# Performance work log

Measured on AMD Instinct MI355X. Metric: run time of the kernel, lower is better.

The kernel has to match this reference:

```python
import jax, jax.numpy as jnp
import numpy as np

N_NODES, N_EDGES, N_GRAPHS, D = 32768, 49152, 1024, 64


def setup_inputs() -> dict:
    key = jax.random.key(0)
    ks = jax.random.split(key, 24)
    p = lambda k, shape, s=0.1: jax.random.normal(k, shape, dtype=jnp.float32) * s
    return dict(
        x=jax.random.normal(ks[0], (N_NODES, 14), dtype=jnp.float32),
        edge_index=jax.random.randint(ks[1], (2, N_EDGES), 0, N_NODES),
        edge_attr=jax.random.uniform(ks[2], (N_EDGES, 4), dtype=jnp.float32),
        batch=jnp.sort(jax.random.randint(ks[3], (N_NODES,), 0, N_GRAPHS)),
        lin0_W=p(ks[4], (D, 14)), lin0_b=p(ks[5], (D,)),
        e1_W=p(ks[6], (128, 4)), e1_b=p(ks[7], (128,)),
        e2_W=p(ks[8], (D * D, 128), 0.02), e2_b=p(ks[9], (D * D,), 0.02),
        root_W=p(ks[10], (D, D)), conv_b=p(ks[11], (D,)),
        gru_Wih=p(ks[12], (3 * D, D)), gru_Whh=p(ks[13], (3 * D, D)),
        gru_bih=p(ks[14], (3 * D,)), gru_bhh=p(ks[15], (3 * D,)),
        lstm_Wih=p(ks[16], (4 * D, 2 * D)), lstm_Whh=p(ks[17], (4 * D, D)),
        lstm_bih=p(ks[18], (4 * D,)), lstm_bhh=p(ks[19], (4 * D,)),
        fc1_W=p(ks[20], (128, 2 * D)), fc1_b=p(ks[21], (128,)),
        fc2_W=p(ks[22], (1, 128)), fc2_b=p(ks[23], (1,)),
    )


def reference(x, edge_index, edge_attr, batch,
              lin0_W, lin0_b, e1_W, e1_b, e2_W, e2_b, root_W, conv_b,
              gru_Wih, gru_Whh, gru_bih, gru_bhh,
              lstm_Wih, lstm_Whh, lstm_bih, lstm_bhh,
              fc1_W, fc1_b, fc2_W, fc2_b):
    N, B = x.shape[0], N_GRAPHS
    src, dst = edge_index[0], edge_index[1]

    out = jax.nn.relu(x @ lin0_W.T + lin0_b)            # [N, D]
    h = out                                             # GRU hidden (num_layers=1)

    # Edge-conditioned weights: edge_attr is constant across the 3 iterations,
    # so compute the edge MLP once (identical math to re-running it).
    W = jax.nn.relu(edge_attr @ e1_W.T + e1_b) @ e2_W.T + e2_b
    W = W.reshape(-1, D, D)                             # [E, D, D]
    cnt = jnp.maximum(
        jax.ops.segment_sum(jnp.ones((src.shape[0],), x.dtype), dst, num_segments=N), 1.0)

    for _ in range(3):
        # NNConv (aggr='mean'): gather -> per-edge matmul -> scatter-mean -> root + bias
        msg = jnp.einsum('ei,eio->eo', out[src], W)     # [E, D]
        agg = jax.ops.segment_sum(msg, dst, num_segments=N) / cnt[:, None]
        m = jax.nn.relu(agg + out @ root_W + conv_b)
        # GRU cell (seq_len=1)
        gi = m @ gru_Wih.T + gru_bih
        gh = h @ gru_Whh.T + gru_bhh
        ir, iz, inn = jnp.split(gi, 3, -1)
        hr, hz, hn = jnp.split(gh, 3, -1)
        r = jax.nn.sigmoid(ir + hr)
        z = jax.nn.sigmoid(iz + hz)
        n = jnp.tanh(inn + r * hn)
        h = (1.0 - z) * n + z * h
        out = h

    # Set2Set pooling, 3 processing steps, LSTM(2D -> D)
    q_star = jnp.zeros((B, 2 * D), x.dtype)
    hl = jnp.zeros((B, D), x.dtype)
    cl = jnp.zeros((B, D), x.dtype)
    for _ in range(3):
        g = q_star @ lstm_Wih.T + lstm_bih + hl @ lstm_Whh.T + lstm_bhh
        i_, f_, g_, o_ = jnp.split(g, 4, -1)
        cl = jax.nn.sigmoid(f_) * cl + jax.nn.sigmoid(i_) * jnp.tanh(g_)
        hl = jax.nn.sigmoid(o_) * jnp.tanh(cl)
        q = hl                                          # [B, D]
        e = jnp.sum(out * q[batch], -1)                 # [N]
        mx = jax.ops.segment_max(e, batch, num_segments=B)
        ex = jnp.exp(e - mx[batch])
        den = jax.ops.segment_sum(ex, batch, num_segments=B)
        a = ex / den[batch]                             # segment softmax
        r_read = jax.ops.segment_sum(a[:, None] * out, batch, num_segments=B)
        q_star = jnp.concatenate([q, r_read], -1)       # [B, 2D]

    hid = jax.nn.relu(q_star @ fc1_W.T + fc1_b)
    return hid @ fc2_W.T + fc2_b                        # [B, 1]
```

## Files before the change

kernel.cpp:

```cpp
#include <hip/hip_runtime.h>
#include <math.h>

#define NN_ 32768
#define NE_ 49152
#define NG_ 1024

typedef short bh8 __attribute__((ext_vector_type(8)));
typedef float f32x4 __attribute__((ext_vector_type(4)));

__device__ __forceinline__ unsigned short f2bfu(float f) {
    union { float f; unsigned int i; } x; x.f = f;
    unsigned int u = x.i;
    u += 0x7FFFu + ((u >> 16) & 1u);
    return (unsigned short)(u >> 16);
}
__device__ __forceinline__ float sigm(float x) { return 1.f / (1.f + expf(-x)); }

__global__ void MPNN_78632261256134_kernel() {}

__global__ void k_init(int* deg, float* agg) {
    int i = blockIdx.x * 256 + threadIdx.x;
    if (i < NN_) deg[i] = 0;
    int k = i - NN_;
    if (k >= 0 && k < NN_ * 64) agg[k] = 0.f;
}

__global__ void k_lin0(const float* x, const float* W, const float* b, float* node) {
    int g = blockIdx.x * 256 + threadIdx.x;
    int n = g >> 6, d = g & 63;
    const float* xr = x + n * 14;
    const float* wr = W + d * 14;
    float acc = b[d];
    for (int i = 0; i < 14; i++) acc += xr[i] * wr[i];
    node[g] = fmaxf(acc, 0.f);
}

__global__ void k_cnt(const int* dst, int* deg) {
    int e = blockIdx.x * 256 + threadIdx.x;
    if (e < NE_) atomicAdd(&deg[dst[e]], 1);
}

__global__ __launch_bounds__(256) void k_scanA(const int* __restrict__ deg,
                                               int* __restrict__ offs,
                                               int* __restrict__ bsum) {
    __shared__ int wtot[4];
    int tid = threadIdx.x, bid = blockIdx.x;
    int i = bid * 256 + tid;
    int v = deg[i];
    int sc = v;
    for (int o = 1; o < 64; o <<= 1) { int u = __shfl_up(sc, o); if ((tid & 63) >= o) sc += u; }
    if ((tid & 63) == 63) wtot[tid >> 6] = sc;
    __syncthreads();
    int wpre = 0;
    for (int k = 0; k < (tid >> 6); k++) wpre += wtot[k];
    offs[i] = sc + wpre - v;
    if (tid == 255) bsum[bid] = sc + wpre;
}

__global__ __launch_bounds__(256) void k_scanC(const int* __restrict__ bsum,
                                               int* __restrict__ offs,
                                               int* __restrict__ head) {
    __shared__ int boff;
    int tid = threadIdx.x, bid = blockIdx.x;
    if (tid == 0) {
        int s = 0;
        for (int k = 0; k < bid; k++) s += bsum[k];
        boff = s;
    }
    __syncthreads();
    int i = bid * 256 + tid;
    int o = offs[i] + boff;
    offs[i] = o; head[i] = o;
    if (i == NN_ - 1) offs[NN_] = NE_;
}

__global__ void k_scatter(const int* __restrict__ dst, int* __restrict__ head,
                          int* __restrict__ perm) {
    int e = blockIdx.x * 256 + threadIdx.x;
    if (e < NE_) { int p = atomicAdd(&head[dst[e]], 1); perm[p] = e; }
}

__global__ void k_gbnd(const int* __restrict__ batch, int* __restrict__ gb) {
    int n = blockIdx.x * 256 + threadIdx.x;
    if (n >= NN_) return;
    int b = batch[n];
    if (n == 0) { for (int g = 0; g <= b; g++) gb[g] = 0; }
    else {
        int pb = batch[n - 1];
        for (int g = pb + 1; g <= b; g++) gb[g] = n;
    }
    if (n == NN_ - 1) { for (int g = b + 1; g <= NG_; g++) gb[g] = NN_; }
}

__global__ void k_tw(const float* gWih, const float* gWhh, float* WihT, float* WhhT,
                     const float* lWih, const float* lWhh, float* WihT2, float* WhhT2,
                     const float* fc1W, float* fc1WT) {
    int t = blockIdx.x * 256 + threadIdx.x;
    if (t < 12288) {
        int gr = t >> 6, i = t & 63; WihT[i * 192 + gr] = gWih[t];
    } else if (t < 24576) {
        int u = t - 12288; int gr = u >> 6, i = u & 63; WhhT[i * 192 + gr] = gWhh[u];
    } else if (t < 57344) {
        int u = t - 24576; int r = u >> 7, c = u & 127; WihT2[c * 256 + r] = lWih[u];
    } else if (t < 73728) {
        int u = t - 57344; int r = u >> 6, c = u & 63; WhhT2[c * 256 + r] = lWhh[u];
    } else if (t < 90112) {
        int u = t - 73728; int r = u >> 7, c = u & 127; fc1WT[c * 128 + r] = fc1W[u];
    }
}

__global__ void k_bhat3(const float* e2W, unsigned short* Bhat3) {
    int idx = blockIdx.x * 256 + threadIdx.x;
    if (idx >= 64 * 4 * 4 * 64 * 8) return;
    int j = idx & 7, lane = (idx >> 3) & 63, t = (idx >> 9) & 3, w = (idx >> 11) & 3, s = idx >> 13;
    int row = s * 64 + w * 16 + (lane & 15);
    int k = t * 32 + (lane >> 4) * 8 + j;
    Bhat3[idx] = f2bfu(e2W[row * 128 + k]);
}

__global__ __launch_bounds__(256) void k_he(const float* __restrict__ ea,
                                            const float* __restrict__ e1W,
                                            const float* __restrict__ e1b,
                                            const int* __restrict__ perm,
                                            unsigned short* __restrict__ Hhat) {
    int tid = threadIdx.x;
    int lane = tid & 63, sub = tid >> 6;
    int gi = blockIdx.x * 4 + sub;
    int etile = gi >> 2, t = gi & 3;
    int e = etile * 16 + (lane & 15), quad = lane >> 4;
    int eo = perm[e];
    const float* ar = ea + (size_t)eo * 4;
    float a0 = ar[0], a1 = ar[1], a2 = ar[2], a3 = ar[3];
    union { unsigned short u[8]; uint4 q; } o;
#pragma unroll
    for (int j = 0; j < 8; j++) {
        int c = t * 32 + quad * 8 + j;
        const float* wr = e1W + c * 4;
        float h = e1b[c] + a0 * wr[0] + a1 * wr[1] + a2 * wr[2] + a3 * wr[3];
        o.u[j] = f2bfu(fmaxf(h, 0.f));
    }
    *(uint4*)(Hhat + (size_t)gi * 512 + lane * 8) = o.q;
}

#define PS(S) (((S) + soff) & 63)

#define LDB(B, S) {                                                                       \
        const unsigned short* _p = Bhat3 + (size_t)PS(S) * 8192 + w * 2048 + lane * 8;    \
        (B)[0] = *(const bh8*)(const void*)(_p);                                          \
        (B)[1] = *(const bh8*)(const void*)(_p + 512);                                    \
        (B)[2] = *(const bh8*)(const void*)(_p + 1024);                                   \
        (B)[3] = *(const bh8*)(const void*)(_p + 1536); }

#define LDXV(XV, S) {                                                                     \
        int sp_ = PS(S);                                                                  \
        _Pragma("unroll")                                                                 \
        for (int mt_ = 0; mt_ < 4; mt_++)                                                 \
            (XV)[mt_] = *(const f32x4*)(const void*)(xs + sp_ * 68 + mt_ * 16 + quad * 4); }

#define LDBB(BB, S) (BB) = e2b[PS(S) * 64 + w * 16 + mrow];

#define MFMA16(ACC, B) {                                                                  \
        __builtin_amdgcn_s_setprio(1);                                                    \
        _Pragma("unroll")                                                                 \
        for (int t_ = 0; t_ < 4; t_++) {                                                  \
            _Pragma("unroll")                                                             \
            for (int mt_ = 0; mt_ < 4; mt_++)                                             \
                (ACC)[mt_] = __builtin_amdgcn_mfma_f32_16x16x32_bf16(                     \
                    af[mt_][t_], (B)[t_], (t_ == 0) ? z4 : (ACC)[mt_], 0, 0, 0);          \
        }                                                                                 \
        __builtin_amdgcn_s_setprio(0); }

#define CONSUME(ACC, XV, BB) {                                                            \
        _Pragma("unroll")                                                                 \
        for (int mt_ = 0; mt_ < 4; mt_++) {                                               \
            _Pragma("unroll")                                                             \
            for (int r_ = 0; r_ < 4; r_++)                                                \
                msgv[mt_][r_] += (XV)[mt_][r_] * ((ACC)[mt_][r_] + (BB));                 \
        } }

__global__ __launch_bounds__(256, 2) void k_convr(const float* __restrict__ node,
                                                  const unsigned short* __restrict__ Hhat,
                                                  const unsigned short* __restrict__ Bhat3,
                                                  const float* __restrict__ e2b,
                                                  const int* __restrict__ src,
                                                  const int* __restrict__ dst,
                                                  const int* __restrict__ perm,
                                                  float* __restrict__ agg) {
    __shared__ __align__(16) float xs[64 * 68];
    __shared__ int dst_s[64];

    const int tid = threadIdx.x;
    const int eb = blockIdx.x * 64;
    const int lane = tid & 63, w = tid >> 6;
    const int quad = lane >> 4, mrow = lane & 15;
    const int soff = (blockIdx.x * 37) & 63;

    {
        int r = tid >> 2, c = tid & 3;
        int s = src[perm[eb + r]];
        const float* nr = node + (size_t)s * 64 + c * 16;
#pragma unroll
        for (int j = 0; j < 16; j++) xs[(c * 16 + j) * 68 + r] = nr[j];
        if (tid < 64) dst_s[tid] = dst[perm[eb + tid]];
    }

    bh8 af[4][4];
#pragma unroll
    for (int mt = 0; mt < 4; mt++)
#pragma unroll
        for (int t = 0; t < 4; t++)
            af[mt][t] = *(const bh8*)(const void*)(
                Hhat + (size_t)(((eb >> 4) + mt) * 4 + t) * 512 + lane * 8);
    __syncthreads();

    const f32x4 z4 = {0.f, 0.f, 0.f, 0.f};
    f32x4 msgv[4];
#pragma unroll
    for (int mt = 0; mt < 4; mt++) msgv[mt] = z4;

    bh8 b0[4], b1[4];
    f32x4 xvA[4], xvB[4];
    f32x4 accA[4], accB[4];
    float bbA, bbB;

    LDB(b0, 0)
    LDB(b1, 1)
    LDXV(xvA, 0)
    LDBB(bbA, 0)
    MFMA16(accA, b0)
    LDB(b0, 2)

#pragma unroll 1
    for (int s = 0; s < 62; s += 2) {
        MFMA16(accB, b1)
        LDB(b1, s + 3)
        LDXV(xvB, s + 1)
        LDBB(bbB, s + 1)
        CONSUME(accA, xvA, bbA)
        MFMA16(accA, b0)
        LDB(b0, (s + 4) & 63)
        LDXV(xvA, s + 2)
        LDBB(bbA, s + 2)
        CONSUME(accB, xvB, bbB)
    }
    MFMA16(accB, b1)
    CONSUME(accA, xvA, bbA)
    LDXV(xvB, 63)
    LDBB(bbB, 63)
    CONSUME(accB, xvB, bbB)

    __syncthreads();
#pragma unroll
    for (int mt = 0; mt < 4; mt++)
#pragma unroll
        for (int r = 0; r < 4; r++)
            xs[(mt * 16 + quad * 4 + r) * 68 + w * 16 + mrow] = msgv[mt][r];
    __syncthreads();
    {
        const int ebase = w * 16;
        const int d = lane;
        float acc = 0.f;
        int startE = ebase;
        int curn = dst_s[ebase];
#pragma unroll
        for (int e = ebase; e < ebase + 16; e++) {
            acc += xs[e * 68 + d];
            int nxt = (e < ebase + 15) ? dst_s[e + 1] : -1;
            if (nxt != curn) {
                float* dp = agg + (size_t)curn * 64 + d;
                if (startE == ebase || e == ebase + 15) atomicAdd(dp, acc);
                else *dp = acc;
                acc = 0.f; startE = e + 1; curn = nxt;
            }
        }
    }
}

__global__ __launch_bounds__(256) void k_mgru(float* __restrict__ agg,
                                              const int* __restrict__ offs,
                                              const float* __restrict__ node,
                                              const float* __restrict__ rootW,
                                              const float* __restrict__ convb,
                                              const float* __restrict__ WihT,
                                              const float* __restrict__ WhhT,
                                              const float* __restrict__ bih,
                                              const float* __restrict__ bhh,
                                              float* __restrict__ hOut) {
    __shared__ __align__(16) float hsT[64][68];
    __shared__ __align__(16) float msT[64][68];
    const int tid = threadIdx.x;
    const int d = tid & 63, sub = tid >> 6;
    const int nb = blockIdx.x * 64;
    const int r0 = sub * 16;
    const int off = (blockIdx.x * 37) & 63;

    {
#pragma unroll
        for (int j4 = 0; j4 < 4; j4++) {
            f32x4 hv;
#pragma unroll
            for (int j = 0; j < 4; j++)
                hv[j] = node[(size_t)(nb + r0 + j4 * 4 + j) * 64 + d];
            *(f32x4*)&hsT[d][r0 + j4 * 4] = hv;
        }
    }
    __syncthreads();

    {
        float root[16];
#pragma unroll
        for (int j = 0; j < 16; j++) root[j] = 0.f;
        for (int ii = 0; ii < 64; ii++) {
            int i = (ii + off) & 63;
            float wv = rootW[i * 64 + d];
#pragma unroll
            for (int j4 = 0; j4 < 4; j4++) {
                f32x4 h4 = *(const f32x4*)&hsT[i][r0 + j4 * 4];
#pragma unroll
                for (int j = 0; j < 4; j++) root[j4 * 4 + j] += h4[j] * wv;
            }
        }
        float cb = convb[d];
#pragma unroll
        for (int j4 = 0; j4 < 4; j4++) {
            f32x4 mval;
#pragma unroll
            for (int j = 0; j < 4; j++) {
                int n = nb + r0 + j4 * 4 + j;
                float dg = (float)(offs[n + 1] - offs[n]);
                float inv = 1.f / fmaxf(dg, 1.f);
                float av = agg[(size_t)n * 64 + d];
                agg[(size_t)n * 64 + d] = 0.f;
                mval[j] = fmaxf(av * inv + cb + root[j4 * 4 + j], 0.f);
            }
            *(f32x4*)&msT[d][r0 + j4 * 4] = mval;
        }
    }
    __syncthreads();

    float ir[16], iz[16], in_[16], hr[16], hz[16], hn[16];
    {
        float bi0 = bih[d], bi1 = bih[64 + d], bi2 = bih[128 + d];
        float bh0 = bhh[d], bh1 = bhh[64 + d], bh2 = bhh[128 + d];
#pragma unroll
        for (int j = 0; j < 16; j++) {
            ir[j] = bi0; iz[j] = bi1; in_[j] = bi2;
            hr[j] = bh0; hz[j] = bh1; hn[j] = bh2;
        }
    }
    for (int ii = 0; ii < 64; ii++) {
        int i = (ii + off) & 63;
        float wi0 = WihT[i * 192 + d];
        float wi1 = WihT[i * 192 + 64 + d];
        float wi2 = WihT[i * 192 + 128 + d];
        float wh0 = WhhT[i * 192 + d];
        float wh1 = WhhT[i * 192 + 64 + d];
        float wh2 = WhhT[i * 192 + 128 + d];
#pragma unroll
        for (int j4 = 0; j4 < 4; j4++) {
            f32x4 m4 = *(const f32x4*)&msT[i][r0 + j4 * 4];
            f32x4 h4 = *(const f32x4*)&hsT[i][r0 + j4 * 4];
#pragma unroll
            for (int j = 0; j < 4; j++) {
                int jj = j4 * 4 + j;
                ir[jj] += m4[j] * wi0; iz[jj] += m4[j] * wi1; in_[jj] += m4[j] * wi2;
                hr[jj] += h4[j] * wh0; hz[jj] += h4[j] * wh1; hn[jj] += h4[j] * wh2;
            }
        }
    }
#pragma unroll
    for (int j = 0; j < 16; j++) {
        float hold = hsT[d][r0 + j];
        float r = sigm(ir[j] + hr[j]);
        float z = sigm(iz[j] + hz[j]);
        float nn = tanhf(in_[j] + r * hn[j]);
        hOut[(size_t)(nb + r0 + j) * 64 + d] = (1.f - z) * nn + z * hold;
    }
}

__global__ __launch_bounds__(256) void k_s2s3(const float* __restrict__ node,
                                              const int* __restrict__ gb,
                                              const float* __restrict__ WihT2,
                                              const float* __restrict__ WhhT2,
                                              const float* __restrict__ bih,
                                              const float* __restrict__ bhh,
                                              float* __restrict__ qstar) {
    __shared__ float qvs[128];
    __shared__ float hls[64], cls[64], qsh[64];
    __shared__ float accs[4][64];
    __shared__ float es[256];
    __shared__ float red[4][64];
    __shared__ float sred[4];
    const int b = blockIdx.x, tid = threadIdx.x;
    const int lane = tid & 63, wv = tid >> 6;
    const int start = gb[b], end = gb[b + 1];

    if (tid < 128) qvs[tid] = 0.f;
    else if (tid < 192) hls[tid - 128] = 0.f;
    else cls[tid - 192] = 0.f;
    __syncthreads();

    for (int step = 0; step < 3; step++) {
        float acc = bih[wv * 64 + lane] + bhh[wv * 64 + lane];
        if (step > 0) {
            const float* wih = WihT2 + wv * 64 + lane;
            const float* whh = WhhT2 + wv * 64 + lane;
#pragma unroll 4
            for (int j = 0; j < 128; j++) acc += qvs[j] * wih[(size_t)j * 256];
#pragma unroll 4
            for (int j = 0; j < 64; j++) acc += hls[j] * whh[(size_t)j * 256];
        }
        accs[wv][lane] = acc;
        __syncthreads();
        if (tid < 64) {
            float c = sigm(accs[1][tid]) * cls[tid] + sigm(accs[0][tid]) * tanhf(accs[2][tid]);
            cls[tid] = c;
            float q = sigm(accs[3][tid]) * tanhf(c);
            hls[tid] = q; qsh[tid] = q;
        }
        __syncthreads();
        const float q = qsh[lane];

        float m_run = -1e30f, l_run = 0.f, r_part = 0.f;
        for (int cbase = start; cbase < end; cbase += 256) {
            int cn = min(256, end - cbase);
            for (int i = wv; i < cn; i += 4) {
                float nv = node[(size_t)(cbase + i) * 64 + lane];
                float p = nv * q;
#pragma unroll
                for (int o = 32; o > 0; o >>= 1) p += __shfl_xor(p, o);
                if (lane == 0) es[i] = p;
            }
            __syncthreads();
            float mloc = -1e30f;
            for (int i = tid; i < cn; i += 256) mloc = fmaxf(mloc, es[i]);
#pragma unroll
            for (int o = 32; o > 0; o >>= 1) mloc = fmaxf(mloc, __shfl_xor(mloc, o));
            if (lane == 0) sred[wv] = mloc;
            __syncthreads();
            float m_chunk = fmaxf(fmaxf(sred[0], sred[1]), fmaxf(sred[2], sred[3]));
            float m_new = fmaxf(m_run, m_chunk);
            float sc = expf(m_run - m_new);
            float lloc = 0.f;
            for (int i = tid; i < cn; i += 256) {
                float wgt = expf(es[i] - m_new);
                es[i] = wgt; lloc += wgt;
            }
#pragma unroll
            for (int o = 32; o > 0; o >>= 1) lloc += __shfl_xor(lloc, o);
            __syncthreads();
            if (lane == 0) sred[wv] = lloc;
            __syncthreads();
            float l_chunk = sred[0] + sred[1] + sred[2] + sred[3];
            l_run = l_run * sc + l_chunk;
            r_part *= sc;
            for (int i = wv; i < cn; i += 4)
                r_part += es[i] * node[(size_t)(cbase + i) * 64 + lane];
            m_run = m_new;
            __syncthreads();
        }
        red[wv][lane] = r_part;
        __syncthreads();
        if (tid < 64) {
            float r = red[0][tid] + red[1][tid] + red[2][tid] + red[3][tid];
            qvs[tid] = qsh[tid];
            qvs[64 + tid] = (end > start) ? r / l_run : 0.f;
        }
        __syncthreads();
    }
    if (tid < 128) qstar[(size_t)b * 128 + tid] = qvs[tid];
}

__global__ void k_fc(const float* qstar, const float* W1T, const float* b1,
                     const float* W2, const float* b2, float* out) {
    __shared__ float hid[128];
    __shared__ float qs[128];
    int b = blockIdx.x; int t = threadIdx.x;
    qs[t] = qstar[(size_t)b * 128 + t];
    __syncthreads();
    float acc = b1[t];
    for (int k = 0; k < 128; k++) acc += qs[k] * W1T[k * 128 + t];
    hid[t] = fmaxf(acc, 0.f);
    __syncthreads();
    if (t < 64) {
        float s = hid[t] * W2[t] + hid[t + 64] * W2[t + 64];
        for (int o = 32; o > 0; o >>= 1) s += __shfl_xor(s, o);
        if (t == 0) out[b] = s + b2[0];
    }
}

extern "C" void kernel_launch(void* const* d_in, const int* in_sizes, int n_in,
                              void* d_out, int out_size, void* d_ws, size_t ws_size,
                              hipStream_t stream) {
    const float* x     = (const float*)d_in[0];
    const int*   ei    = (const int*)d_in[1];
    const float* ea    = (const float*)d_in[2];
    const int*   batch = (const int*)d_in[3];
    const float* lin0W = (const float*)d_in[4];
    const float* lin0b = (const float*)d_in[5];
    const float* e1W   = (const float*)d_in[6];
    const float* e1b   = (const float*)d_in[7];
    const float* e2W   = (const float*)d_in[8];
    const float* e2b   = (const float*)d_in[9];
    const float* rootW = (const float*)d_in[10];
    const float* convb = (const float*)d_in[11];
    const float* gWih  = (const float*)d_in[12];
    const float* gWhh  = (const float*)d_in[13];
    const float* gbih  = (const float*)d_in[14];
    const float* gbhh  = (const float*)d_in[15];
    const float* lWih  = (const float*)d_in[16];
    const float* lWhh  = (const float*)d_in[17];
    const float* lbih  = (const float*)d_in[18];
    const float* lbhh  = (const float*)d_in[19];
    const float* fc1W  = (const float*)d_in[20];
    const float* fc1b  = (const float*)d_in[21];
    const float* fc2W  = (const float*)d_in[22];
    const float* fc2b  = (const float*)d_in[23];
    const int* src = ei;
    const int* dst = ei + NE_;

    char* p = (char*)d_ws;
    auto alloc = [&](size_t bytes) -> char* {
        char* r = p; p += (bytes + 255) & ~(size_t)255; return r;
    };
    unsigned short* Bhat3 = (unsigned short*)alloc((size_t)524288 * 2);
    unsigned short* Hhat  = (unsigned short*)alloc((size_t)NE_ * 128 * 2);
    float* nodeA  = (float*)alloc((size_t)NN_ * 64 * 4);
    float* nodeB  = (float*)alloc((size_t)NN_ * 64 * 4);
    float* aggb   = (float*)alloc((size_t)NN_ * 64 * 4);
    int*   deg    = (int*)alloc((size_t)NN_ * 4);
    int*   offs   = (int*)alloc((size_t)(NN_ + 1) * 4);
    int*   head   = (int*)alloc((size_t)NN_ * 4);
    int*   perm   = (int*)alloc((size_t)NE_ * 4);
    int*   bsum   = (int*)alloc((size_t)128 * 4);
    int*   gb     = (int*)alloc((size_t)(NG_ + 1) * 4);
    float* WihT   = (float*)alloc(192 * 64 * 4);
    float* WhhT   = (float*)alloc(192 * 64 * 4);
    float* WihT2  = (float*)alloc(256 * 128 * 4);
    float* WhhT2  = (float*)alloc(256 * 64 * 4);
    float* fc1WT  = (float*)alloc(128 * 128 * 4);
    float* qstar  = (float*)alloc((size_t)NG_ * 128 * 4);

    k_init<<<(NN_ + NN_ * 64 + 255) / 256, 256, 0, stream>>>(deg, aggb);
    k_lin0<<<NN_ * 64 / 256, 256, 0, stream>>>(x, lin0W, lin0b, nodeA);
    k_cnt<<<NE_ / 256, 256, 0, stream>>>(dst, deg);
    k_scanA<<<NN_ / 256, 256, 0, stream>>>(deg, offs, bsum);
    k_scanC<<<NN_ / 256, 256, 0, stream>>>(bsum, offs, head);
    k_scatter<<<NE_ / 256, 256, 0, stream>>>(dst, head, perm);
    k_gbnd<<<NN_ / 256, 256, 0, stream>>>(batch, gb);
    k_tw<<<352, 256, 0, stream>>>(gWih, gWhh, WihT, WhhT, lWih, lWhh, WihT2, WhhT2,
                                  fc1W, fc1WT);
    k_bhat3<<<524288 / 256, 256, 0, stream>>>(e2W, Bhat3);
    k_he<<<NE_ / 16, 256, 0, stream>>>(ea, e1W, e1b, perm, Hhat);

    float* curF = nodeA; float* nxtF = nodeB;
    for (int it = 0; it < 3; it++) {
        k_convr<<<NE_ / 64, 256, 0, stream>>>(curF, Hhat, Bhat3, e2b, src, dst, perm, aggb);
        k_mgru<<<NN_ / 64, 256, 0, stream>>>(aggb, offs, curF, rootW, convb,
                                             WihT, WhhT, gbih, gbhh, nxtF);
        float* tf = curF; curF = nxtF; nxtF = tf;
    }

    k_s2s3<<<NG_, 256, 0, stream>>>(curF, gb, WihT2, WhhT2, lbih, lbhh, qstar);
    k_fc<<<NG_, 128, 0, stream>>>(qstar, fc1WT, fc1b, fc2W, fc2b, (float*)d_out);
}
```

Baseline: 444.4 us.

## Double the threads in the GRU kernel and stage GRU weights through LDS

The fused root+GRU kernel now runs 512 threads per 64-node block, with each thread handling 8 nodes instead of 16. GRU input and hidden weight rows are staged into a double-buffered shared-memory tile in chunks of 8 rows, replacing direct per-thread global loads. The root-weight loop also prefetches the next row in software. Halving the per-thread accumulators cuts register pressure and adds parallelism, at the cost of more shared memory and eight block-wide barriers.

After: 465.7 us. 4.8% more time.

```diff
diff --git a/kernel.cpp b/kernel.cpp
--- a/kernel.cpp
+++ b/kernel.cpp
@@ -276,7 +276,7 @@
     }
 }
 
-__global__ __launch_bounds__(256) void k_mgru(float* __restrict__ agg,
+__global__ __launch_bounds__(512) void k_mgru(float* __restrict__ agg,
                                               const int* __restrict__ offs,
                                               const float* __restrict__ node,
                                               const float* __restrict__ rootW,
@@ -288,15 +288,15 @@
                                               float* __restrict__ hOut) {
     __shared__ __align__(16) float hsT[64][68];
     __shared__ __align__(16) float msT[64][68];
+    __shared__ __align__(16) float ws[2][8][384];
     const int tid = threadIdx.x;
     const int d = tid & 63, sub = tid >> 6;
     const int nb = blockIdx.x * 64;
-    const int r0 = sub * 16;
-    const int off = (blockIdx.x * 37) & 63;
+    const int r0 = sub * 8;
 
     {
 #pragma unroll
-        for (int j4 = 0; j4 < 4; j4++) {
+        for (int j4 = 0; j4 < 2; j4++) {
             f32x4 hv;
 #pragma unroll
             for (int j = 0; j < 4; j++)
@@ -307,22 +307,31 @@
     __syncthreads();
 
     {
-        float root[16];
-#pragma unroll
-        for (int j = 0; j < 16; j++) root[j] = 0.f;
-        for (int ii = 0; ii < 64; ii++) {
-            int i = (ii + off) & 63;
-            float wv = rootW[i * 64 + d];
-#pragma unroll
-            for (int j4 = 0; j4 < 4; j4++) {
-                f32x4 h4 = *(const f32x4*)&hsT[i][r0 + j4 * 4];
-#pragma unroll
-                for (int j = 0; j < 4; j++) root[j4 * 4 + j] += h4[j] * wv;
-            }
+        const float* wi = WihT + (size_t)sub * 192;
+        const float* wh = WhhT + (size_t)sub * 192;
+#pragma unroll
+        for (int j = 0; j < 3; j++) {
+            ws[0][sub][d + 64 * j] = wi[d + 64 * j];
+            ws[0][sub][192 + d + 64 * j] = wh[d + 64 * j];
+        }
+    }
+
+    {
+        float root[8];
+#pragma unroll
+        for (int j = 0; j < 8; j++) root[j] = 0.f;
+        float wv = rootW[d];
+        for (int i = 0; i < 64; i++) {
+            float wn = rootW[((i + 1) & 63) * 64 + d];
+            f32x4 h4a = *(const f32x4*)&hsT[i][r0];
+            f32x4 h4b = *(const f32x4*)&hsT[i][r0 + 4];
+#pragma unroll
+            for (int j = 0; j < 4; j++) { root[j] += h4a[j] * wv; root[4 + j] += h4b[j] * wv; }
+            wv = wn;
         }
         float cb = convb[d];
 #pragma unroll
-        for (int j4 = 0; j4 < 4; j4++) {
+        for (int j4 = 0; j4 < 2; j4++) {
             f32x4 mval;
 #pragma unroll
             for (int j = 0; j < 4; j++) {
@@ -338,38 +347,56 @@
     }
     __syncthreads();
 
-    float ir[16], iz[16], in_[16], hr[16], hz[16], hn[16];
+    float ir[8], iz[8], in_[8], hr[8], hz[8], hn[8];
     {
         float bi0 = bih[d], bi1 = bih[64 + d], bi2 = bih[128 + d];
         float bh0 = bhh[d], bh1 = bhh[64 + d], bh2 = bhh[128 + d];
 #pragma unroll
-        for (int j = 0; j < 16; j++) {
+        for (int j = 0; j < 8; j++) {
             ir[j] = bi0; iz[j] = bi1; in_[j] = bi2;
             hr[j] = bh0; hz[j] = bh1; hn[j] = bh2;
         }
     }
-    for (int ii = 0; ii < 64; ii++) {
-        int i = (ii + off) & 63;
-        float wi0 = WihT[i * 192 + d];
-        float wi1 = WihT[i * 192 + 64 + d];
-        float wi2 = WihT[i * 192 + 128 + d];
-        float wh0 = WhhT[i * 192 + d];
-        float wh1 = WhhT[i * 192 + 64 + d];
-        float wh2 = WhhT[i * 192 + 128 + d];
-#pragma unroll
-        for (int j4 = 0; j4 < 4; j4++) {
-            f32x4 m4 = *(const f32x4*)&msT[i][r0 + j4 * 4];
-            f32x4 h4 = *(const f32x4*)&hsT[i][r0 + j4 * 4];
+
+#pragma unroll 1
+    for (int c = 0; c < 8; c++) {
+        int buf = c & 1;
+        if (c < 7) {
+            int i = (c + 1) * 8 + sub;
+            const float* wi = WihT + (size_t)i * 192;
+            const float* wh = WhhT + (size_t)i * 192;
+#pragma unroll
+            for (int j = 0; j < 3; j++) {
+                ws[buf ^ 1][sub][d + 64 * j] = wi[d + 64 * j];
+                ws[buf ^ 1][sub][192 + d + 64 * j] = wh[d + 64 * j];
+            }
+        }
+#pragma unroll
+        for (int k = 0; k < 8; k++) {
+            int i = c * 8 + k;
+            float wi0 = ws[buf][k][d];
+            float wi1 = ws[buf][k][64 + d];
+            float wi2 = ws[buf][k][128 + d];
+            float wh0 = ws[buf][k][192 + d];
+            float wh1 = ws[buf][k][256 + d];
+            float wh2 = ws[buf][k][320 + d];
+            f32x4 m4a = *(const f32x4*)&msT[i][r0];
+            f32x4 m4b = *(const f32x4*)&msT[i][r0 + 4];
+            f32x4 h4a = *(const f32x4*)&hsT[i][r0];
+            f32x4 h4b = *(const f32x4*)&hsT[i][r0 + 4];
 #pragma unroll
             for (int j = 0; j < 4; j++) {
-                int jj = j4 * 4 + j;
-                ir[jj] += m4[j] * wi0; iz[jj] += m4[j] * wi1; in_[jj] += m4[j] * wi2;
-                hr[jj] += h4[j] * wh0; hz[jj] += h4[j] * wh1; hn[jj] += h4[j] * wh2;
+                ir[j] += m4a[j] * wi0; iz[j] += m4a[j] * wi1; in_[j] += m4a[j] * wi2;
+                hr[j] += h4a[j] * wh0; hz[j] += h4a[j] * wh1; hn[j] += h4a[j] * wh2;
+                ir[4 + j] += m4b[j] * wi0; iz[4 + j] += m4b[j] * wi1; in_[4 + j] += m4b[j] * wi2;
+                hr[4 + j] += h4b[j] * wh0; hz[4 + j] += h4b[j] * wh1; hn[4 + j] += h4b[j] * wh2;
             }
         }
-    }
-#pragma unroll
-    for (int j = 0; j < 16; j++) {
+        __syncthreads();
+    }
+
+#pragma unroll
+    for (int j = 0; j < 8; j++) {
         float hold = hsT[d][r0 + j];
         float r = sigm(ir[j] + hr[j]);
         float z = sigm(iz[j] + hz[j]);
@@ -556,7 +583,7 @@
     float* curF = nodeA; float* nxtF = nodeB;
     for (int it = 0; it < 3; it++) {
         k_convr<<<NE_ / 64, 256, 0, stream>>>(curF, Hhat, Bhat3, e2b, src, dst, perm, aggb);
-        k_mgru<<<NN_ / 64, 256, 0, stream>>>(aggb, offs, curF, rootW, convb,
+        k_mgru<<<NN_ / 64, 512, 0, stream>>>(aggb, offs, curF, rootW, convb,
                                              WihT, WhhT, gbih, gbhh, nxtF);
         float* tf = curF; curF = nxtF; nxtF = tf;
     }
```

## Run GRU and root matmuls in k_mgru on MFMA with split-bf16 precision

Applied to the files above, without the earlier changes.

Replaces the scalar FP32 FMA loops in the fused NNConv-root/GRU kernel with bf16 MFMA 16x16x32 instructions. Each FP32 operand is split into bf16 hi and lo parts and three MFMAs per tile recover near-FP32 accuracy. A new preprocessing kernel packs Whh concatenated with rootW, and Wih, into MFMA B-fragment layout as hi/lo bf16 pairs. This removes a large FP32 ALU cost, in exchange for extra conversion work, register pressure and a small precision loss.

Measured after the change: 425.2 us. 4.3% less time.

```diff
diff --git a/kernel.cpp b/kernel.cpp
--- a/kernel.cpp
+++ b/kernel.cpp
@@ -92,21 +92,49 @@
     if (n == NN_ - 1) { for (int g = b + 1; g <= NG_; g++) gb[g] = NN_; }
 }
 
-__global__ void k_tw(const float* gWih, const float* gWhh, float* WihT, float* WhhT,
-                     const float* lWih, const float* lWhh, float* WihT2, float* WhhT2,
+__global__ void k_tw(const float* lWih, const float* lWhh, float* WihT2, float* WhhT2,
                      const float* fc1W, float* fc1WT) {
     int t = blockIdx.x * 256 + threadIdx.x;
-    if (t < 12288) {
-        int gr = t >> 6, i = t & 63; WihT[i * 192 + gr] = gWih[t];
-    } else if (t < 24576) {
-        int u = t - 12288; int gr = u >> 6, i = u & 63; WhhT[i * 192 + gr] = gWhh[u];
-    } else if (t < 57344) {
-        int u = t - 24576; int r = u >> 7, c = u & 127; WihT2[c * 256 + r] = lWih[u];
-    } else if (t < 73728) {
-        int u = t - 57344; int r = u >> 6, c = u & 63; WhhT2[c * 256 + r] = lWhh[u];
-    } else if (t < 90112) {
-        int u = t - 73728; int r = u >> 7, c = u & 127; fc1WT[c * 128 + r] = fc1W[u];
-    }
+    if (t < 32768) {
+        int r = t >> 7, cc = t & 127; WihT2[cc * 256 + r] = lWih[t];
+    } else if (t < 49152) {
+        int u = t - 32768; int r = u >> 6, cc = u & 63; WhhT2[cc * 256 + r] = lWhh[u];
+    } else if (t < 65536) {
+        int u = t - 49152; int r = u >> 7, cc = u & 127; fc1WT[cc * 128 + r] = fc1W[u];
+    }
+}
+
+__global__ void k_wfrag(const float* __restrict__ gWih, const float* __restrict__ gWhh,
+                        const float* __restrict__ rootW,
+                        unsigned short* __restrict__ HHh, unsigned short* __restrict__ HHl,
+                        unsigned short* __restrict__ IHh, unsigned short* __restrict__ IHl) {
+    int idx = blockIdx.x * 256 + threadIdx.x;
+    if (idx >= 28672) return;
+    float w;
+    unsigned short *oh, *ol;
+    if (idx < 16384) {
+        int f = idx;
+        int tile = f >> 9, within = f & 511;
+        int l = within >> 3, j = within & 7;
+        int ot = tile >> 1, kt = tile & 1;
+        int col = ot * 16 + (l & 15);
+        int k = kt * 32 + (l >> 4) * 8 + j;
+        w = (col < 192) ? gWhh[col * 64 + k] : rootW[k * 64 + (col - 192)];
+        oh = HHh + f; ol = HHl + f;
+    } else {
+        int f = idx - 16384;
+        int tile = f >> 9, within = f & 511;
+        int l = within >> 3, j = within & 7;
+        int ot = tile >> 1, kt = tile & 1;
+        int col = ot * 16 + (l & 15);
+        int k = kt * 32 + (l >> 4) * 8 + j;
+        w = gWih[col * 64 + k];
+        oh = IHh + f; ol = IHl + f;
+    }
+    unsigned short hi = f2bfu(w);
+    union { unsigned int i; float f; } hv; hv.i = (unsigned int)hi << 16;
+    unsigned short lo = f2bfu(w - hv.f);
+    *oh = hi; *ol = lo;
 }
 
 __global__ void k_bhat3(const float* e2W, unsigned short* Bhat3) {
@@ -279,102 +307,121 @@
 __global__ __launch_bounds__(256) void k_mgru(float* __restrict__ agg,
                                               const int* __restrict__ offs,
                                               const float* __restrict__ node,
-                                              const float* __restrict__ rootW,
+                                              const unsigned short* __restrict__ HHh,
+                                              const unsigned short* __restrict__ HHl,
+                                              const unsigned short* __restrict__ IHh,
+                                              const unsigned short* __restrict__ IHl,
                                               const float* __restrict__ convb,
-                                              const float* __restrict__ WihT,
-                                              const float* __restrict__ WhhT,
                                               const float* __restrict__ bih,
                                               const float* __restrict__ bhh,
                                               float* __restrict__ hOut) {
-    __shared__ __align__(16) float hsT[64][68];
-    __shared__ __align__(16) float msT[64][68];
+    __shared__ __align__(16) float hs[64][68];
+    __shared__ __align__(16) float ms[64][68];
     const int tid = threadIdx.x;
-    const int d = tid & 63, sub = tid >> 6;
+    const int lane = tid & 63, wvt = tid >> 6;
+    const int quad = lane >> 4, c = lane & 15;
     const int nb = blockIdx.x * 64;
-    const int r0 = sub * 16;
-    const int off = (blockIdx.x * 37) & 63;
+    const f32x4 z4 = {0.f, 0.f, 0.f, 0.f};
 
     {
-#pragma unroll
-        for (int j4 = 0; j4 < 4; j4++) {
-            f32x4 hv;
-#pragma unroll
-            for (int j = 0; j < 4; j++)
-                hv[j] = node[(size_t)(nb + r0 + j4 * 4 + j) * 64 + d];
-            *(f32x4*)&hsT[d][r0 + j4 * 4] = hv;
-        }
-    }
-    __syncthreads();
-
-    {
-        float root[16];
-#pragma unroll
-        for (int j = 0; j < 16; j++) root[j] = 0.f;
-        for (int ii = 0; ii < 64; ii++) {
-            int i = (ii + off) & 63;
-            float wv = rootW[i * 64 + d];
-#pragma unroll
-            for (int j4 = 0; j4 < 4; j4++) {
-                f32x4 h4 = *(const f32x4*)&hsT[i][r0 + j4 * 4];
-#pragma unroll
-                for (int j = 0; j < 4; j++) root[j4 * 4 + j] += h4[j] * wv;
-            }
-        }
-        float cb = convb[d];
-#pragma unroll
-        for (int j4 = 0; j4 < 4; j4++) {
-            f32x4 mval;
-#pragma unroll
-            for (int j = 0; j < 4; j++) {
-                int n = nb + r0 + j4 * 4 + j;
-                float dg = (float)(offs[n + 1] - offs[n]);
-                float inv = 1.f / fmaxf(dg, 1.f);
-                float av = agg[(size_t)n * 64 + d];
-                agg[(size_t)n * 64 + d] = 0.f;
-                mval[j] = fmaxf(av * inv + cb + root[j4 * 4 + j], 0.f);
-            }
-            *(f32x4*)&msT[d][r0 + j4 * 4] = mval;
-        }
-    }
-    __syncthreads();
-
-    float ir[16], iz[16], in_[16], hr[16], hz[16], hn[16];
-    {
-        float bi0 = bih[d], bi1 = bih[64 + d], bi2 = bih[128 + d];
-        float bh0 = bhh[d], bh1 = bhh[64 + d], bh2 = bhh[128 + d];
-#pragma unroll
-        for (int j = 0; j < 16; j++) {
-            ir[j] = bi0; iz[j] = bi1; in_[j] = bi2;
-            hr[j] = bh0; hz[j] = bh1; hn[j] = bh2;
-        }
-    }
-    for (int ii = 0; ii < 64; ii++) {
-        int i = (ii + off) & 63;
-        float wi0 = WihT[i * 192 + d];
-        float wi1 = WihT[i * 192 + 64 + d];
-        float wi2 = WihT[i * 192 + 128 + d];
-        float wh0 = WhhT[i * 192 + d];
-        float wh1 = WhhT[i * 192 + 64 + d];
-        float wh2 = WhhT[i * 192 + 128 + d];
-#pragma unroll
-        for (int j4 = 0; j4 < 4; j4++) {
-            f32x4 m4 = *(const f32x4*)&msT[i][r0 + j4 * 4];
-            f32x4 h4 = *(const f32x4*)&hsT[i][r0 + j4 * 4];
-#pragma unroll
-            for (int j = 0; j < 4; j++) {
-                int jj = j4 * 4 + j;
-                ir[jj] += m4[j] * wi0; iz[jj] += m4[j] * wi1; in_[jj] += m4[j] * wi2;
-                hr[jj] += h4[j] * wh0; hz[jj] += h4[j] * wh1; hn[jj] += h4[j] * wh2;
-            }
-        }
-    }
-#pragma unroll
-    for (int j = 0; j < 16; j++) {
-        float hold = hsT[d][r0 + j];
-        float r = sigm(ir[j] + hr[j]);
-        float z = sigm(iz[j] + hz[j]);
-        float nn = tanhf(in_[j] + r * hn[j]);
-        hOut[(size_t)(nb + r0 + j) * 64 + d] = (1.f - z) * nn + z * hold;
+        int n = tid >> 2, dc = (tid & 3) * 16;
+        const float* nr = node + (size_t)(nb + n) * 64 + dc;
+#pragma unroll
+        for (int j4 = 0; j4 < 4; j4++)
+            *(f32x4*)&hs[n][dc + j4 * 4] = *(const f32x4*)(nr + j4 * 4);
+    }
+    __syncthreads();
+
+    bh8 ah[2], al[2];
+#pragma unroll
+    for (int kt = 0; kt < 2; kt++) {
+#pragma unroll
+        for (int j = 0; j < 8; j++) {
+            float x = hs[wvt * 16 + c][kt * 32 + quad * 8 + j];
+            unsigned short h = f2bfu(x);
+            union { unsigned int i; float f; } hv; hv.i = (unsigned int)h << 16;
+            unsigned short l = f2bfu(x - hv.f);
+            ah[kt][j] = (short)h; al[kt][j] = (short)l;
+        }
+    }
+
+    f32x4 hacc[16];
+#pragma unroll
+    for (int ot = 0; ot < 16; ot++) {
+        f32x4 a = z4;
+#pragma unroll
+        for (int kt = 0; kt < 2; kt++) {
+            bh8 bh = *(const bh8*)(const void*)(HHh + (ot * 2 + kt) * 512 + lane * 8);
+            bh8 bl = *(const bh8*)(const void*)(HHl + (ot * 2 + kt) * 512 + lane * 8);
+            a = __builtin_amdgcn_mfma_f32_16x16x32_bf16(ah[kt], bh, a, 0, 0, 0);
+            a = __builtin_amdgcn_mfma_f32_16x16x32_bf16(ah[kt], bl, a, 0, 0, 0);
+            a = __builtin_amdgcn_mfma_f32_16x16x32_bf16(al[kt], bh, a, 0, 0, 0);
+        }
+        hacc[ot] = a;
+    }
+
+    int nrow[4]; float invd[4];
+#pragma unroll
+    for (int r = 0; r < 4; r++) {
+        nrow[r] = nb + wvt * 16 + quad * 4 + r;
+        int dg = offs[nrow[r] + 1] - offs[nrow[r]];
+        invd[r] = 1.f / fmaxf((float)dg, 1.f);
+    }
+#pragma unroll
+    for (int k = 0; k < 4; k++) {
+        float cb = convb[c + 16 * k];
+#pragma unroll
+        for (int r = 0; r < 4; r++) {
+            size_t ai = (size_t)nrow[r] * 64 + c + 16 * k;
+            float m = fmaxf(agg[ai] * invd[r] + cb + hacc[12 + k][r], 0.f);
+            agg[ai] = 0.f;
+            ms[wvt * 16 + quad * 4 + r][c + 16 * k] = m;
+        }
+    }
+    __syncthreads();
+
+    bh8 amh[2], aml[2];
+#pragma unroll
+    for (int kt = 0; kt < 2; kt++) {
+#pragma unroll
+        for (int j = 0; j < 8; j++) {
+            float x = ms[wvt * 16 + c][kt * 32 + quad * 8 + j];
+            unsigned short h = f2bfu(x);
+            union { unsigned int i; float f; } hv; hv.i = (unsigned int)h << 16;
+            unsigned short l = f2bfu(x - hv.f);
+            amh[kt][j] = (short)h; aml[kt][j] = (short)l;
+        }
+    }
+
+    f32x4 macc[12];
+#pragma unroll
+    for (int ot = 0; ot < 12; ot++) {
+        f32x4 a = z4;
+#pragma unroll
+        for (int kt = 0; kt < 2; kt++) {
+            bh8 bh = *(const bh8*)(const void*)(IHh + (ot * 2 + kt) * 512 + lane * 8);
+            bh8 bl = *(const bh8*)(const void*)(IHl + (ot * 2 + kt) * 512 + lane * 8);
+            a = __builtin_amdgcn_mfma_f32_16x16x32_bf16(amh[kt], bh, a, 0, 0, 0);
+            a = __builtin_amdgcn_mfma_f32_16x16x32_bf16(amh[kt], bl, a, 0, 0, 0);
+            a = __builtin_amdgcn_mfma_f32_16x16x32_bf16(aml[kt], bh, a, 0, 0, 0);
+        }
+        macc[ot] = a;
+    }
+
+#pragma unroll
+    for (int k = 0; k < 4; k++) {
+        int d = c + 16 * k;
+        float bir = bih[d], biz = bih[64 + d], bin = bih[128 + d];
+        float bhr = bhh[d], bhz = bhh[64 + d], bhn = bhh[128 + d];
+#pragma unroll
+        for (int r = 0; r < 4; r++) {
+            float rr = sigm(macc[k][r] + bir + hacc[k][r] + bhr);
+            float zz = sigm(macc[4 + k][r] + biz + hacc[4 + k][r] + bhz);
+            float hnv = hacc[8 + k][r] + bhn;
+            float nn = tanhf(macc[8 + k][r] + bin + rr * hnv);
+            float hold = hs[wvt * 16 + quad * 4 + r][d];
+            hOut[(size_t)nrow[r] * 64 + d] = (1.f - zz) * nn + zz * hold;
+        }
     }
 }
 
@@ -534,8 +581,10 @@
     int*   perm   = (int*)alloc((size_t)NE_ * 4);
     int*   bsum   = (int*)alloc((size_t)128 * 4);
     int*   gb     = (int*)alloc((size_t)(NG_ + 1) * 4);
-    float* WihT   = (float*)alloc(192 * 64 * 4);
-    float* WhhT   = (float*)alloc(192 * 64 * 4);
+    unsigned short* HHh = (unsigned short*)alloc((size_t)16384 * 2);
+    unsigned short* HHl = (unsigned short*)alloc((size_t)16384 * 2);
+    unsigned short* IHh = (unsigned short*)alloc((size_t)12288 * 2);
+    unsigned short* IHl = (unsigned short*)alloc((size_t)12288 * 2);
     float* WihT2  = (float*)alloc(256 * 128 * 4);
     float* WhhT2  = (float*)alloc(256 * 64 * 4);
     float* fc1WT  = (float*)alloc(128 * 128 * 4);
@@ -548,16 +597,16 @@
     k_scanC<<<NN_ / 256, 256, 0, stream>>>(bsum, offs, head);
     k_scatter<<<NE_ / 256, 256, 0, stream>>>(dst, head, perm);
     k_gbnd<<<NN_ / 256, 256, 0, stream>>>(batch, gb);
-    k_tw<<<352, 256, 0, stream>>>(gWih, gWhh, WihT, WhhT, lWih, lWhh, WihT2, WhhT2,
-                                  fc1W, fc1WT);
+    k_tw<<<256, 256, 0, stream>>>(lWih, lWhh, WihT2, WhhT2, fc1W, fc1WT);
+    k_wfrag<<<112, 256, 0, stream>>>(gWih, gWhh, rootW, HHh, HHl, IHh, IHl);
     k_bhat3<<<524288 / 256, 256, 0, stream>>>(e2W, Bhat3);
     k_he<<<NE_ / 16, 256, 0, stream>>>(ea, e1W, e1b, perm, Hhat);
 
     float* curF = nodeA; float* nxtF = nodeB;
     for (int it = 0; it < 3; it++) {
         k_convr<<<NE_ / 64, 256, 0, stream>>>(curF, Hhat, Bhat3, e2b, src, dst, perm, aggb);
-        k_mgru<<<NN_ / 64, 256, 0, stream>>>(aggb, offs, curF, rootW, convb,
-                                             WihT, WhhT, gbih, gbhh, nxtF);
+        k_mgru<<<NN_ / 64, 256, 0, stream>>>(aggb, offs, curF, HHh, HHl, IHh, IHl,
+                                             convb, gbih, gbhh, nxtF);
         float* tf = curF; curF = nxtF; nxtF = tf;
     }
 
```
